# Kernel optimization log

Hardware: AMD Instinct MI355X
Metric: run time of the kernel (lower is better)

Reference implementation:

```python
import jax, jax.numpy as jnp
import numpy as np


def _glorot(key, shape):
    fan_in, fan_out = shape[0], shape[1]
    lim = np.sqrt(6.0 / (fan_in + fan_out))
    return jax.random.uniform(key, shape, jnp.float32, -lim, lim)


def setup_inputs() -> dict:
    key = jax.random.key(0)
    ks = jax.random.split(key, 32)
    B, NR, NT = 16384, 64, 128
    inp = {
        "tier0_features": jax.random.normal(ks[0], (B, 44), jnp.float32),
        "robot_features": jax.random.normal(ks[1], (B, NR, 6), jnp.float32),
        "track_features": jax.random.normal(ks[2], (B, NT, 7), jnp.float32),
        # robot SetEncoder: 6 -> 64 -> 64 -> 32
        "rw1": _glorot(ks[3], (6, 64)),  "rb1": jnp.zeros((64,), jnp.float32),
        "rw2": _glorot(ks[4], (64, 64)), "rb2": jnp.zeros((64,), jnp.float32),
        "rw3": _glorot(ks[5], (64, 32)), "rb3": jnp.zeros((32,), jnp.float32),
        # track SetEncoder: 7 -> 64 -> 64 -> 32
        "tw1": _glorot(ks[6], (7, 64)),  "tb1": jnp.zeros((64,), jnp.float32),
        "tw2": _glorot(ks[7], (64, 64)), "tb2": jnp.zeros((64,), jnp.float32),
        "tw3": _glorot(ks[8], (64, 32)), "tb3": jnp.zeros((32,), jnp.float32),
        # head MLP: 108 -> 128 -> 128 -> 64 -> 1
        "mw1": _glorot(ks[9], (108, 128)),  "mb1": jnp.zeros((128,), jnp.float32),
        "mw2": _glorot(ks[10], (128, 128)), "mb2": jnp.zeros((128,), jnp.float32),
        "mw3": _glorot(ks[11], (128, 64)),  "mb3": jnp.zeros((64,), jnp.float32),
        "mw4": _glorot(ks[12], (64, 1)),    "mb4": jnp.zeros((1,), jnp.float32),
    }
    return inp


def _set_encode(x, w1, b1, w2, b2, w3, b3):
    # x: [B, N, d_in] -> pooled [B, 32]; mask=None path: mean+max over set dim
    h = jax.nn.relu(jnp.einsum('bnd,dh->bnh', x, w1) + b1)
    h = jax.nn.relu(jnp.einsum('bnh,hk->bnk', h, w2) + b2)
    e = jnp.einsum('bnk,ko->bno', h, w3) + b3
    return (e.mean(axis=1) + e.max(axis=1)) * 0.5


def reference(tier0_features, robot_features, track_features,
              rw1, rb1, rw2, rb2, rw3, rb3,
              tw1, tb1, tw2, tb2, tw3, tb3,
              mw1, mb1, mw2, mb2, mw3, mb3, mw4, mb4):
    robot_emb = _set_encode(robot_features, rw1, rb1, rw2, rb2, rw3, rb3)  # [B,32]
    track_emb = _set_encode(track_features, tw1, tb1, tw2, tb2, tw3, tb3)  # [B,32]
    c = jnp.concatenate([tier0_features, robot_emb, track_emb], axis=1)    # [B,108]
    h = jax.nn.relu(c @ mw1 + mb1)
    h = jax.nn.relu(h @ mw2 + mb2)
    h = jax.nn.relu(h @ mw3 + mb3)
    return (h @ mw4 + mb4).squeeze(-1)  # [B]
```

## Files before the change

kernel.cpp:

```cpp
#include <hip/hip_runtime.h>
#include <hip/hip_bf16.h>

#define DEV_INLINE __device__ __forceinline__

typedef __bf16 bf16x8 __attribute__((ext_vector_type(8)));
typedef float  floatx4 __attribute__((ext_vector_type(4)));

DEV_INLINE bf16x8 ld_frag(const __bf16* p) {
    union { uint4 u; bf16x8 v; } t;
    t.u = *(const uint4*)p;
    return t.v;
}
DEV_INLINE bf16x8 pack_relu2(floatx4 a, floatx4 b) {
    float2 p0 = {fmaxf(a[0], 0.0f), fmaxf(a[1], 0.0f)};
    float2 p1 = {fmaxf(a[2], 0.0f), fmaxf(a[3], 0.0f)};
    float2 p2 = {fmaxf(b[0], 0.0f), fmaxf(b[1], 0.0f)};
    float2 p3 = {fmaxf(b[2], 0.0f), fmaxf(b[3], 0.0f)};
    union { __hip_bfloat162 h[4]; bf16x8 v; } t;
    t.h[0] = __float22bfloat162_rn(p0);
    t.h[1] = __float22bfloat162_rn(p1);
    t.h[2] = __float22bfloat162_rn(p2);
    t.h[3] = __float22bfloat162_rn(p3);
    return t.v;
}
DEV_INLINE floatx4 vmax4(floatx4 a, floatx4 b) {
    floatx4 r;
#pragma unroll
    for (int i = 0; i < 4; ++i) r[i] = fmaxf(a[i], b[i]);
    return r;
}

template<int N, int Kp, int Ks>
DEV_INLINE void tp(__bf16* dst, const float* __restrict__ src, int idx0, int stride) {
    for (int e = idx0; e < N * Kp; e += stride) {
        int n = e / Kp, k = e - n * Kp;
        dst[e] = (k < Ks) ? (__bf16)src[k * N + n] : (__bf16)0.0f;
    }
}
template<int N, int K>
DEV_INLINE void tp_perm(__bf16* dst, const float* __restrict__ src, int idx0, int stride) {
    for (int e = idx0; e < N * K; e += stride) {
        int n = e / K, kh = e - n * K;
        int qd = (kh >> 3) & 3, kq = kh >> 5, j = kh & 7;
        int c = (2 * kq + (j >> 2)) * 16 + qd * 4 + (j & 3);
        dst[e] = (__bf16)src[c * N + n];
    }
}

__global__ __launch_bounds__(256)
void prep_kernel(const float* __restrict__ rw1, const float* __restrict__ rw2,
                 const float* __restrict__ rw3,
                 const float* __restrict__ tw1, const float* __restrict__ tw2,
                 const float* __restrict__ tw3,
                 const float* __restrict__ mw1, const float* __restrict__ mw2,
                 const float* __restrict__ mw3, __bf16* __restrict__ wb)
{
    int i0 = blockIdx.x * 256 + threadIdx.x;
    int st = gridDim.x * 256;
    tp     < 64,  32,   6>(wb + 0,     rw1, i0, st);
    tp_perm< 64,  64>     (wb + 2048,  rw2, i0, st);
    tp_perm< 32,  64>     (wb + 6144,  rw3, i0, st);
    tp     < 64,  32,   7>(wb + 8192,  tw1, i0, st);
    tp_perm< 64,  64>     (wb + 10240, tw2, i0, st);
    tp_perm< 32,  64>     (wb + 14336, tw3, i0, st);
    tp     <128, 128, 108>(wb + 16384, mw1, i0, st);
    tp_perm<128, 128>     (wb + 32768, mw2, i0, st);
    tp_perm< 64, 128>     (wb + 49152, mw3, i0, st);
}

struct __align__(16) EncSmem {
    float e3s[64 * 36];
    float e3m[64 * 36];
    float pool[512];
    float bs[160];
};

template<int DIN, int S, int ITERS>
DEV_INLINE void enc_loop(EncSmem& sm, const float* __restrict__ X,
                         const __bf16* __restrict__ w1p,
                         const __bf16* __restrict__ w2p,
                         const __bf16* __restrict__ w3p,
                         const float* __restrict__ b1, const float* __restrict__ b2,
                         const float* __restrict__ b3,
                         __bf16* __restrict__ out, int bid0)
{
    constexpr int NB = 128 / S;
    const int tid = threadIdx.x;
    const int w   = tid >> 6;
    const int l64 = tid & 63;
    const int ln  = l64 & 15;
    const int qd  = l64 >> 4;

    if (tid < 160)
        sm.bs[tid] = (tid < 64) ? b1[tid]
                   : (tid < 128) ? b2[tid - 64] : b3[tid - 128];

    bf16x8 w1f[4], w2f[4][2], w3f[2][2];
#pragma unroll
    for (int mt = 0; mt < 4; ++mt)
        w1f[mt] = ld_frag(&w1p[(mt * 16 + ln) * 32 + qd * 8]);
#pragma unroll
    for (int mt = 0; mt < 4; ++mt)
#pragma unroll
        for (int kq = 0; kq < 2; ++kq)
            w2f[mt][kq] = ld_frag(&w2p[(mt * 16 + ln) * 64 + kq * 32 + qd * 8]);
#pragma unroll
    for (int mt = 0; mt < 2; ++mt)
#pragma unroll
        for (int kq = 0; kq < 2; ++kq)
            w3f[mt][kq] = ld_frag(&w3p[(mt * 16 + ln) * 64 + kq * 32 + qd * 8]);
    __syncthreads();

    for (int it = 0; it < ITERS; ++it) {
        const int bid = bid0 + it;

        bf16x8 xb[2];
#pragma unroll
        for (int t = 0; t < 2; ++t) {
            bf16x8 v;
#pragma unroll
            for (int j = 0; j < 8; ++j) v[j] = (__bf16)0.0f;
            if (qd == 0) {
                const int row = (2 * w + t) * 16 + ln;
                const float* xp = X + ((size_t)bid * 128 + row) * DIN;
#pragma unroll
                for (int j = 0; j < DIN; ++j) v[j] = (__bf16)xp[j];
            }
            xb[t] = v;
        }
        floatx4 a1[2][4];
#pragma unroll
        for (int mt = 0; mt < 4; ++mt) {
            float4 bv = *(const float4*)&sm.bs[mt * 16 + qd * 4];
#pragma unroll
            for (int t = 0; t < 2; ++t) {
                floatx4 acc = (floatx4){bv.x, bv.y, bv.z, bv.w};
                a1[t][mt] = __builtin_amdgcn_mfma_f32_16x16x32_bf16(w1f[mt], xb[t], acc, 0, 0, 0);
            }
        }
        bf16x8 f1[2][2];
#pragma unroll
        for (int t = 0; t < 2; ++t)
#pragma unroll
            for (int kq = 0; kq < 2; ++kq)
                f1[t][kq] = pack_relu2(a1[t][2 * kq], a1[t][2 * kq + 1]);

        floatx4 a2[2][4];
#pragma unroll
        for (int mt = 0; mt < 4; ++mt) {
            float4 bv = *(const float4*)&sm.bs[64 + mt * 16 + qd * 4];
#pragma unroll
            for (int t = 0; t < 2; ++t) {
                floatx4 acc = (floatx4){bv.x, bv.y, bv.z, bv.w};
                acc = __builtin_amdgcn_mfma_f32_16x16x32_bf16(w2f[mt][0], f1[t][0], acc, 0, 0, 0);
                acc = __builtin_amdgcn_mfma_f32_16x16x32_bf16(w2f[mt][1], f1[t][1], acc, 0, 0, 0);
                a2[t][mt] = acc;
            }
        }
        bf16x8 f2[2][2];
#pragma unroll
        for (int t = 0; t < 2; ++t)
#pragma unroll
            for (int kq = 0; kq < 2; ++kq)
                f2[t][kq] = pack_relu2(a2[t][2 * kq], a2[t][2 * kq + 1]);

        floatx4 a3[2][2];
#pragma unroll
        for (int mt = 0; mt < 2; ++mt) {
            float4 bv = *(const float4*)&sm.bs[128 + mt * 16 + qd * 4];
#pragma unroll
            for (int t = 0; t < 2; ++t) {
                floatx4 acc = (floatx4){bv.x, bv.y, bv.z, bv.w};
                acc = __builtin_amdgcn_mfma_f32_16x16x32_bf16(w3f[mt][0], f2[t][0], acc, 0, 0, 0);
                acc = __builtin_amdgcn_mfma_f32_16x16x32_bf16(w3f[mt][1], f2[t][1], acc, 0, 0, 0);
                a3[t][mt] = acc;
            }
        }
#pragma unroll
        for (int mt = 0; mt < 2; ++mt) {
            floatx4 s = a3[0][mt] + a3[1][mt];
            floatx4 m = vmax4(a3[0][mt], a3[1][mt]);
            float4 so = {s[0], s[1], s[2], s[3]};
            float4 mo = {m[0], m[1], m[2], m[3]};
            *(float4*)&sm.e3s[(w * 16 + ln) * 36 + mt * 16 + qd * 4] = so;
            *(float4*)&sm.e3m[(w * 16 + ln) * 36 + mt * 16 + qd * 4] = mo;
        }
        __syncthreads();

        {
            constexpr int R = 64 / NB;
            const int o  = tid & 31;
            const int bi = (tid >> 5) % NB;
            const int ch = tid / (32 * NB);
            const int p0 = bi * R + ch * 8;
            float s = 0.0f, m = -3.4e38f;
#pragma unroll
            for (int r = 0; r < 8; ++r) {
                s += sm.e3s[(p0 + r) * 36 + o];
                m = fmaxf(m, sm.e3m[(p0 + r) * 36 + o]);
            }
            sm.pool[tid] = s;
            sm.pool[256 + tid] = m;
        }
        __syncthreads();
        if (tid < NB * 32) {
            constexpr int C = 8 / NB;
            float s = 0.0f, m = -3.4e38f;
#pragma unroll
            for (int c = 0; c < C; ++c) {
                s += sm.pool[tid + c * 32 * NB];
                m = fmaxf(m, sm.pool[256 + tid + c * 32 * NB]);
            }
            size_t b = (size_t)bid * NB + (tid >> 5);
            out[b * 32 + (tid & 31)] = (__bf16)(0.5f * (s * (1.0f / S) + m));
        }
    }
}

__global__ __launch_bounds__(256, 3)
void enc_fused(const float* __restrict__ rX, const float* __restrict__ tX,
               const __bf16* __restrict__ wb,
               const float* __restrict__ rb1, const float* __restrict__ rb2,
               const float* __restrict__ rb3,
               const float* __restrict__ tb1, const float* __restrict__ tb2,
               const float* __restrict__ tb3,
               __bf16* __restrict__ remb, __bf16* __restrict__ temb)
{
    __shared__ EncSmem sm;
    if ((int)blockIdx.x < 256)
        enc_loop<6, 64, 32>(sm, rX, wb, wb + 2048, wb + 6144,
                            rb1, rb2, rb3, remb, blockIdx.x * 32);
    else
        enc_loop<7, 128, 32>(sm, tX, wb + 8192, wb + 10240, wb + 14336,
                             tb1, tb2, tb3, temb, (blockIdx.x - 256) * 32);
}

__global__ __launch_bounds__(256)
void head_mfma(const float* __restrict__ t0,
               const __bf16* __restrict__ remb, const __bf16* __restrict__ temb,
               const __bf16* __restrict__ hw1, const float* __restrict__ b1,
               const __bf16* __restrict__ hw2, const float* __restrict__ b2,
               const __bf16* __restrict__ hw3, const float* __restrict__ b3,
               const float* __restrict__ w4, const float* __restrict__ b4,
               float* __restrict__ out)
{
    __shared__ __align__(16) __bf16 cb[64 * 136];

    const int tid = threadIdx.x;
    const int w   = tid >> 6;
    const int l64 = tid & 63;
    const int ln  = l64 & 15;
    const int qd  = l64 >> 4;
    const int g0  = blockIdx.x * 64;

    for (int i = tid; i < 64 * 44; i += 256) {
        int r = i / 44, k = i - r * 44;
        cb[r * 136 + k] = (__bf16)t0[(size_t)(g0 + r) * 44 + k];
    }
    for (int i = tid; i < 64 * 32; i += 256) {
        int r = i >> 5, k = i & 31;
        cb[r * 136 + 44 + k] = remb[(size_t)(g0 + r) * 32 + k];
        cb[r * 136 + 76 + k] = temb[(size_t)(g0 + r) * 32 + k];
    }
    for (int i = tid; i < 64 * 20; i += 256) {
        int r = i / 20, k = i - r * 20;
        cb[r * 136 + 108 + k] = (__bf16)0.0f;
    }
    __syncthreads();

    bf16x8 cf[4];
#pragma unroll
    for (int kq = 0; kq < 4; ++kq)
        cf[kq] = ld_frag(&cb[(w * 16 + ln) * 136 + kq * 32 + qd * 8]);
    floatx4 acc1[8];
#pragma unroll
    for (int mt = 0; mt < 8; ++mt) {
        float4 bv = *(const float4*)&b1[mt * 16 + qd * 4];
        floatx4 acc = (floatx4){bv.x, bv.y, bv.z, bv.w};
#pragma unroll
        for (int kq = 0; kq < 4; ++kq) {
            bf16x8 af = ld_frag(&hw1[(mt * 16 + ln) * 128 + kq * 32 + qd * 8]);
            acc = __builtin_amdgcn_mfma_f32_16x16x32_bf16(af, cf[kq], acc, 0, 0, 0);
        }
        acc1[mt] = acc;
    }
    bf16x8 f1[4];
#pragma unroll
    for (int kq = 0; kq < 4; ++kq)
        f1[kq] = pack_relu2(acc1[2 * kq], acc1[2 * kq + 1]);

    floatx4 acc2[8];
#pragma unroll
    for (int mt = 0; mt < 8; ++mt) {
        float4 bv = *(const float4*)&b2[mt * 16 + qd * 4];
        floatx4 acc = (floatx4){bv.x, bv.y, bv.z, bv.w};
#pragma unroll
        for (int kq = 0; kq < 4; ++kq) {
            bf16x8 af = ld_frag(&hw2[(mt * 16 + ln) * 128 + kq * 32 + qd * 8]);
            acc = __builtin_amdgcn_mfma_f32_16x16x32_bf16(af, f1[kq], acc, 0, 0, 0);
        }
        acc2[mt] = acc;
    }
    bf16x8 f2[4];
#pragma unroll
    for (int kq = 0; kq < 4; ++kq)
        f2[kq] = pack_relu2(acc2[2 * kq], acc2[2 * kq + 1]);

    floatx4 acc3[4];
#pragma unroll
    for (int mt = 0; mt < 4; ++mt) {
        float4 bv = *(const float4*)&b3[mt * 16 + qd * 4];
        floatx4 acc = (floatx4){bv.x, bv.y, bv.z, bv.w};
#pragma unroll
        for (int kq = 0; kq < 4; ++kq) {
            bf16x8 af = ld_frag(&hw3[(mt * 16 + ln) * 128 + kq * 32 + qd * 8]);
            acc = __builtin_amdgcn_mfma_f32_16x16x32_bf16(af, f2[kq], acc, 0, 0, 0);
        }
        acc3[mt] = acc;
    }

    float part = 0.0f;
#pragma unroll
    for (int mt = 0; mt < 4; ++mt) {
        float4 wv = *(const float4*)&w4[mt * 16 + qd * 4];
        part = fmaf(fmaxf(acc3[mt][0], 0.0f), wv.x, part);
        part = fmaf(fmaxf(acc3[mt][1], 0.0f), wv.y, part);
        part = fmaf(fmaxf(acc3[mt][2], 0.0f), wv.z, part);
        part = fmaf(fmaxf(acc3[mt][3], 0.0f), wv.w, part);
    }
    part += __shfl_xor(part, 16);
    part += __shfl_xor(part, 32);
    if (qd == 0)
        out[g0 + w * 16 + ln] = part + b4[0];
}

extern "C" void kernel_launch(void* const* d_in, const int* in_sizes, int n_in,
                              void* d_out, int out_size, void* d_ws, size_t ws_size,
                              hipStream_t stream)
{
    const float* t0  = (const float*)d_in[0];
    const float* rX  = (const float*)d_in[1];
    const float* tX  = (const float*)d_in[2];
    const float* rw1 = (const float*)d_in[3];  const float* rb1 = (const float*)d_in[4];
    const float* rw2 = (const float*)d_in[5];  const float* rb2 = (const float*)d_in[6];
    const float* rw3 = (const float*)d_in[7];  const float* rb3 = (const float*)d_in[8];
    const float* tw1 = (const float*)d_in[9];  const float* tb1 = (const float*)d_in[10];
    const float* tw2 = (const float*)d_in[11]; const float* tb2 = (const float*)d_in[12];
    const float* tw3 = (const float*)d_in[13]; const float* tb3 = (const float*)d_in[14];
    const float* mw1 = (const float*)d_in[15]; const float* mb1 = (const float*)d_in[16];
    const float* mw2 = (const float*)d_in[17]; const float* mb2 = (const float*)d_in[18];
    const float* mw3 = (const float*)d_in[19]; const float* mb3 = (const float*)d_in[20];
    const float* mw4 = (const float*)d_in[21]; const float* mb4 = (const float*)d_in[22];
    float* out = (float*)d_out;

    const int B = 16384;
    __bf16* remb = (__bf16*)d_ws;
    __bf16* temb = (__bf16*)((char*)d_ws + ((size_t)1 << 20));
    __bf16* wb   = (__bf16*)((char*)d_ws + ((size_t)2 << 20));
    const __bf16* mw1b = wb + 16384; const __bf16* mw2b = wb + 32768;
    const __bf16* mw3b = wb + 49152;

    prep_kernel<<<64, 256, 0, stream>>>(rw1, rw2, rw3, tw1, tw2, tw3,
                                        mw1, mw2, mw3, wb);
    enc_fused<<<768, 256, 0, stream>>>(rX, tX, wb,
                                       rb1, rb2, rb3, tb1, tb2, tb3,
                                       remb, temb);
    head_mfma<<<B / 64, 256, 0, stream>>>(t0, remb, temb,
                                          mw1b, mb1, mw2b, mb2, mw3b, mb3,
                                          mw4, mb4, out);
}
```

Measured before the change: 238.6 us.

## Restructure set encoders to one wave per batch with in-register pooling

Each wavefront now processes whole batch elements, with a grid-stride loop over the batch. Mean/max pooling is done in registers, using cross-lane shuffles instead of shared memory and block barriers. The first-layer bias is folded into the padded weight column by appending a constant 1 to the input, and the next tile's input is prefetched during compute. Grid sizes are rebalanced so track blocks get twice as many as robot blocks. This removes the LDS traffic and __syncthreads, but adds shuffle work and raises register pressure, and launch_bounds no longer requests 3 blocks per CU.

Result: slower. 315.9 us (+32.4%).

```diff
diff --git a/kernel.cpp b/kernel.cpp
--- a/kernel.cpp
+++ b/kernel.cpp
@@ -23,18 +23,21 @@
     t.h[3] = __float22bfloat162_rn(p3);
     return t.v;
 }
-DEV_INLINE floatx4 vmax4(floatx4 a, floatx4 b) {
-    floatx4 r;
-#pragma unroll
-    for (int i = 0; i < 4; ++i) r[i] = fmaxf(a[i], b[i]);
-    return r;
-}
 
 template<int N, int Kp, int Ks>
 DEV_INLINE void tp(__bf16* dst, const float* __restrict__ src, int idx0, int stride) {
     for (int e = idx0; e < N * Kp; e += stride) {
         int n = e / Kp, k = e - n * Kp;
         dst[e] = (k < Ks) ? (__bf16)src[k * N + n] : (__bf16)0.0f;
+    }
+}
+template<int N, int Kp, int Ks>
+DEV_INLINE void tp_bias(__bf16* dst, const float* __restrict__ src,
+                        const float* __restrict__ bias, int idx0, int stride) {
+    for (int e = idx0; e < N * Kp; e += stride) {
+        int n = e / Kp, k = e - n * Kp;
+        dst[e] = (k < Ks) ? (__bf16)src[k * N + n]
+               : (k == Ks) ? (__bf16)bias[n] : (__bf16)0.0f;
     }
 }
 template<int N, int K>
@@ -48,19 +51,19 @@
 }
 
 __global__ __launch_bounds__(256)
-void prep_kernel(const float* __restrict__ rw1, const float* __restrict__ rw2,
-                 const float* __restrict__ rw3,
-                 const float* __restrict__ tw1, const float* __restrict__ tw2,
-                 const float* __restrict__ tw3,
+void prep_kernel(const float* __restrict__ rw1, const float* __restrict__ rb1,
+                 const float* __restrict__ rw2, const float* __restrict__ rw3,
+                 const float* __restrict__ tw1, const float* __restrict__ tb1,
+                 const float* __restrict__ tw2, const float* __restrict__ tw3,
                  const float* __restrict__ mw1, const float* __restrict__ mw2,
                  const float* __restrict__ mw3, __bf16* __restrict__ wb)
 {
     int i0 = blockIdx.x * 256 + threadIdx.x;
     int st = gridDim.x * 256;
-    tp     < 64,  32,   6>(wb + 0,     rw1, i0, st);
+    tp_bias< 64,  32,   6>(wb + 0,     rw1, rb1, i0, st);
     tp_perm< 64,  64>     (wb + 2048,  rw2, i0, st);
     tp_perm< 32,  64>     (wb + 6144,  rw3, i0, st);
-    tp     < 64,  32,   7>(wb + 8192,  tw1, i0, st);
+    tp_bias< 64,  32,   7>(wb + 8192,  tw1, tb1, i0, st);
     tp_perm< 64,  64>     (wb + 10240, tw2, i0, st);
     tp_perm< 32,  64>     (wb + 14336, tw3, i0, st);
     tp     <128, 128, 108>(wb + 16384, mw1, i0, st);
@@ -68,33 +71,21 @@
     tp_perm< 64, 128>     (wb + 49152, mw3, i0, st);
 }
 
-struct __align__(16) EncSmem {
-    float e3s[64 * 36];
-    float e3m[64 * 36];
-    float pool[512];
-    float bs[160];
-};
-
-template<int DIN, int S, int ITERS>
-DEV_INLINE void enc_loop(EncSmem& sm, const float* __restrict__ X,
+template<int DIN, int S, int GPB>
+DEV_INLINE void enc_wave(const float* __restrict__ X,
                          const __bf16* __restrict__ w1p,
                          const __bf16* __restrict__ w2p,
                          const __bf16* __restrict__ w3p,
-                         const float* __restrict__ b1, const float* __restrict__ b2,
+                         const float* __restrict__ b2,
                          const float* __restrict__ b3,
-                         __bf16* __restrict__ out, int bid0)
-{
-    constexpr int NB = 128 / S;
-    const int tid = threadIdx.x;
-    const int w   = tid >> 6;
-    const int l64 = tid & 63;
+                         __bf16* __restrict__ out,
+                         int wid, int nw)
+{
+    constexpr int NBATCH = 16384;
+    const int l64 = threadIdx.x & 63;
     const int ln  = l64 & 15;
     const int qd  = l64 >> 4;
 
-    if (tid < 160)
-        sm.bs[tid] = (tid < 64) ? b1[tid]
-                   : (tid < 128) ? b2[tid - 64] : b3[tid - 128];
-
     bf16x8 w1f[4], w2f[4][2], w3f[2][2];
 #pragma unroll
     for (int mt = 0; mt < 4; ++mt)
@@ -109,130 +100,141 @@
 #pragma unroll
         for (int kq = 0; kq < 2; ++kq)
             w3f[mt][kq] = ld_frag(&w3p[(mt * 16 + ln) * 64 + kq * 32 + qd * 8]);
-    __syncthreads();
-
-    for (int it = 0; it < ITERS; ++it) {
-        const int bid = bid0 + it;
-
-        bf16x8 xb[2];
+    float4 bv2[4], bv3[2];
+#pragma unroll
+    for (int mt = 0; mt < 4; ++mt) bv2[mt] = *(const float4*)&b2[mt * 16 + qd * 4];
+#pragma unroll
+    for (int mt = 0; mt < 2; ++mt) bv3[mt] = *(const float4*)&b3[mt * 16 + qd * 4];
+
+    auto load_x = [&](int b, int g, bf16x8 xb[2]) {
 #pragma unroll
         for (int t = 0; t < 2; ++t) {
             bf16x8 v;
 #pragma unroll
             for (int j = 0; j < 8; ++j) v[j] = (__bf16)0.0f;
             if (qd == 0) {
-                const int row = (2 * w + t) * 16 + ln;
-                const float* xp = X + ((size_t)bid * 128 + row) * DIN;
+                const float* xp = X + ((size_t)b * S + (2 * g + t) * 16 + ln) * DIN;
 #pragma unroll
                 for (int j = 0; j < DIN; ++j) v[j] = (__bf16)xp[j];
+                v[DIN] = (__bf16)1.0f;
             }
             xb[t] = v;
         }
-        floatx4 a1[2][4];
-#pragma unroll
-        for (int mt = 0; mt < 4; ++mt) {
-            float4 bv = *(const float4*)&sm.bs[mt * 16 + qd * 4];
-#pragma unroll
-            for (int t = 0; t < 2; ++t) {
-                floatx4 acc = (floatx4){bv.x, bv.y, bv.z, bv.w};
-                a1[t][mt] = __builtin_amdgcn_mfma_f32_16x16x32_bf16(w1f[mt], xb[t], acc, 0, 0, 0);
-            }
-        }
-        bf16x8 f1[2][2];
-#pragma unroll
-        for (int t = 0; t < 2; ++t)
-#pragma unroll
-            for (int kq = 0; kq < 2; ++kq)
-                f1[t][kq] = pack_relu2(a1[t][2 * kq], a1[t][2 * kq + 1]);
-
-        floatx4 a2[2][4];
-#pragma unroll
-        for (int mt = 0; mt < 4; ++mt) {
-            float4 bv = *(const float4*)&sm.bs[64 + mt * 16 + qd * 4];
-#pragma unroll
-            for (int t = 0; t < 2; ++t) {
-                floatx4 acc = (floatx4){bv.x, bv.y, bv.z, bv.w};
-                acc = __builtin_amdgcn_mfma_f32_16x16x32_bf16(w2f[mt][0], f1[t][0], acc, 0, 0, 0);
-                acc = __builtin_amdgcn_mfma_f32_16x16x32_bf16(w2f[mt][1], f1[t][1], acc, 0, 0, 0);
-                a2[t][mt] = acc;
-            }
-        }
-        bf16x8 f2[2][2];
-#pragma unroll
-        for (int t = 0; t < 2; ++t)
-#pragma unroll
-            for (int kq = 0; kq < 2; ++kq)
-                f2[t][kq] = pack_relu2(a2[t][2 * kq], a2[t][2 * kq + 1]);
-
-        floatx4 a3[2][2];
+    };
+
+    if (wid >= NBATCH) return;
+    bf16x8 xc[2];
+    load_x(wid, 0, xc);
+
+    for (int b = wid; b < NBATCH; b += nw) {
+        floatx4 s[2], m[2];
 #pragma unroll
         for (int mt = 0; mt < 2; ++mt) {
-            float4 bv = *(const float4*)&sm.bs[128 + mt * 16 + qd * 4];
-#pragma unroll
-            for (int t = 0; t < 2; ++t) {
-                floatx4 acc = (floatx4){bv.x, bv.y, bv.z, bv.w};
-                acc = __builtin_amdgcn_mfma_f32_16x16x32_bf16(w3f[mt][0], f2[t][0], acc, 0, 0, 0);
-                acc = __builtin_amdgcn_mfma_f32_16x16x32_bf16(w3f[mt][1], f2[t][1], acc, 0, 0, 0);
-                a3[t][mt] = acc;
-            }
-        }
-#pragma unroll
-        for (int mt = 0; mt < 2; ++mt) {
-            floatx4 s = a3[0][mt] + a3[1][mt];
-            floatx4 m = vmax4(a3[0][mt], a3[1][mt]);
-            float4 so = {s[0], s[1], s[2], s[3]};
-            float4 mo = {m[0], m[1], m[2], m[3]};
-            *(float4*)&sm.e3s[(w * 16 + ln) * 36 + mt * 16 + qd * 4] = so;
-            *(float4*)&sm.e3m[(w * 16 + ln) * 36 + mt * 16 + qd * 4] = mo;
-        }
-        __syncthreads();
-
-        {
-            constexpr int R = 64 / NB;
-            const int o  = tid & 31;
-            const int bi = (tid >> 5) % NB;
-            const int ch = tid / (32 * NB);
-            const int p0 = bi * R + ch * 8;
-            float s = 0.0f, m = -3.4e38f;
-#pragma unroll
-            for (int r = 0; r < 8; ++r) {
-                s += sm.e3s[(p0 + r) * 36 + o];
-                m = fmaxf(m, sm.e3m[(p0 + r) * 36 + o]);
-            }
-            sm.pool[tid] = s;
-            sm.pool[256 + tid] = m;
-        }
-        __syncthreads();
-        if (tid < NB * 32) {
-            constexpr int C = 8 / NB;
-            float s = 0.0f, m = -3.4e38f;
-#pragma unroll
-            for (int c = 0; c < C; ++c) {
-                s += sm.pool[tid + c * 32 * NB];
-                m = fmaxf(m, sm.pool[256 + tid + c * 32 * NB]);
-            }
-            size_t b = (size_t)bid * NB + (tid >> 5);
-            out[b * 32 + (tid & 31)] = (__bf16)(0.5f * (s * (1.0f / S) + m));
-        }
-    }
-}
-
-__global__ __launch_bounds__(256, 3)
+            s[mt] = (floatx4){0.0f, 0.0f, 0.0f, 0.0f};
+            m[mt] = (floatx4){-3.4e38f, -3.4e38f, -3.4e38f, -3.4e38f};
+        }
+#pragma unroll
+        for (int g = 0; g < GPB; ++g) {
+            floatx4 a1[2][4];
+#pragma unroll
+            for (int mt = 0; mt < 4; ++mt) {
+                floatx4 z = (floatx4){0.0f, 0.0f, 0.0f, 0.0f};
+#pragma unroll
+                for (int t = 0; t < 2; ++t)
+                    a1[t][mt] = __builtin_amdgcn_mfma_f32_16x16x32_bf16(w1f[mt], xc[t], z, 0, 0, 0);
+            }
+            bf16x8 xn[2];
+            {
+                int nb = b, ng = g + 1;
+                if (ng == GPB) { ng = 0; nb = b + nw; if (nb >= NBATCH) nb = b; }
+                load_x(nb, ng, xn);
+            }
+            bf16x8 f1[2][2];
+#pragma unroll
+            for (int t = 0; t < 2; ++t)
+#pragma unroll
+                for (int kq = 0; kq < 2; ++kq)
+                    f1[t][kq] = pack_relu2(a1[t][2 * kq], a1[t][2 * kq + 1]);
+
+            floatx4 a2[2][4];
+#pragma unroll
+            for (int mt = 0; mt < 4; ++mt) {
+                floatx4 bi = (floatx4){bv2[mt].x, bv2[mt].y, bv2[mt].z, bv2[mt].w};
+#pragma unroll
+                for (int t = 0; t < 2; ++t) {
+                    floatx4 acc = bi;
+                    acc = __builtin_amdgcn_mfma_f32_16x16x32_bf16(w2f[mt][0], f1[t][0], acc, 0, 0, 0);
+                    acc = __builtin_amdgcn_mfma_f32_16x16x32_bf16(w2f[mt][1], f1[t][1], acc, 0, 0, 0);
+                    a2[t][mt] = acc;
+                }
+            }
+            bf16x8 f2[2][2];
+#pragma unroll
+            for (int t = 0; t < 2; ++t)
+#pragma unroll
+                for (int kq = 0; kq < 2; ++kq)
+                    f2[t][kq] = pack_relu2(a2[t][2 * kq], a2[t][2 * kq + 1]);
+
+#pragma unroll
+            for (int mt = 0; mt < 2; ++mt) {
+                floatx4 bi = (floatx4){bv3[mt].x, bv3[mt].y, bv3[mt].z, bv3[mt].w};
+#pragma unroll
+                for (int t = 0; t < 2; ++t) {
+                    floatx4 acc = bi;
+                    acc = __builtin_amdgcn_mfma_f32_16x16x32_bf16(w3f[mt][0], f2[t][0], acc, 0, 0, 0);
+                    acc = __builtin_amdgcn_mfma_f32_16x16x32_bf16(w3f[mt][1], f2[t][1], acc, 0, 0, 0);
+                    s[mt] = s[mt] + acc;
+#pragma unroll
+                    for (int j = 0; j < 4; ++j) m[mt][j] = fmaxf(m[mt][j], acc[j]);
+                }
+            }
+            xc[0] = xn[0]; xc[1] = xn[1];
+        }
+#pragma unroll
+        for (int d = 1; d < 16; d <<= 1) {
+#pragma unroll
+            for (int mt = 0; mt < 2; ++mt)
+#pragma unroll
+                for (int j = 0; j < 4; ++j) {
+                    s[mt][j] += __shfl_xor(s[mt][j], d, 64);
+                    float o = __shfl_xor(m[mt][j], d, 64);
+                    m[mt][j] = fmaxf(m[mt][j], o);
+                }
+        }
+        if (ln == 0) {
+            constexpr float invS = 1.0f / (float)S;
+#pragma unroll
+            for (int mt = 0; mt < 2; ++mt) {
+                union { __bf16 h[4]; uint2 u; } o;
+#pragma unroll
+                for (int j = 0; j < 4; ++j)
+                    o.h[j] = (__bf16)(0.5f * (s[mt][j] * invS + m[mt][j]));
+                *(uint2*)&out[(size_t)b * 32 + mt * 16 + qd * 4] = o.u;
+            }
+        }
+    }
+}
+
+#define NRB 341
+#define NTB 683
+
+__global__ __launch_bounds__(256)
 void enc_fused(const float* __restrict__ rX, const float* __restrict__ tX,
                const __bf16* __restrict__ wb,
-               const float* __restrict__ rb1, const float* __restrict__ rb2,
-               const float* __restrict__ rb3,
-               const float* __restrict__ tb1, const float* __restrict__ tb2,
-               const float* __restrict__ tb3,
+               const float* __restrict__ rb2, const float* __restrict__ rb3,
+               const float* __restrict__ tb2, const float* __restrict__ tb3,
                __bf16* __restrict__ remb, __bf16* __restrict__ temb)
 {
-    __shared__ EncSmem sm;
-    if ((int)blockIdx.x < 256)
-        enc_loop<6, 64, 32>(sm, rX, wb, wb + 2048, wb + 6144,
-                            rb1, rb2, rb3, remb, blockIdx.x * 32);
-    else
-        enc_loop<7, 128, 32>(sm, tX, wb + 8192, wb + 10240, wb + 14336,
-                             tb1, tb2, tb3, temb, (blockIdx.x - 256) * 32);
+    const int w = threadIdx.x >> 6;
+    if ((int)blockIdx.x < NRB) {
+        int wid = blockIdx.x * 4 + w;
+        enc_wave<6, 64, 2>(rX, wb, wb + 2048, wb + 6144,
+                           rb2, rb3, remb, wid, NRB * 4);
+    } else {
+        int wid = (blockIdx.x - NRB) * 4 + w;
+        enc_wave<7, 128, 4>(tX, wb + 8192, wb + 10240, wb + 14336,
+                            tb2, tb3, temb, wid, NTB * 4);
+    }
 }
 
 __global__ __launch_bounds__(256)
@@ -360,11 +362,10 @@
     const __bf16* mw1b = wb + 16384; const __bf16* mw2b = wb + 32768;
     const __bf16* mw3b = wb + 49152;
 
-    prep_kernel<<<64, 256, 0, stream>>>(rw1, rw2, rw3, tw1, tw2, tw3,
+    prep_kernel<<<64, 256, 0, stream>>>(rw1, rb1, rw2, rw3, tw1, tb1, tw2, tw3,
                                         mw1, mw2, mw3, wb);
-    enc_fused<<<768, 256, 0, stream>>>(rX, tX, wb,
-                                       rb1, rb2, rb3, tb1, tb2, tb3,
-                                       remb, temb);
+    enc_fused<<<NRB + NTB, 256, 0, stream>>>(rX, tX, wb,
+                                             rb2, rb3, tb2, tb3, remb, temb);
     head_mfma<<<B / 64, 256, 0, stream>>>(t0, remb, temb,
                                           mw1b, mb1, mw2b, mb2, mw3b, mb3,
                                           mw4, mb4, out);
```
